# Kernel optimization log

Hardware: AMD Instinct MI355X
Metric: run time of the kernel (lower is better)

The kernel has to match this reference:

```python
import jax, jax.numpy as jnp
import numpy as np

# ---- constants (from init_kwargs / Box defaults) ----
B, K, T = 32768, 256, 10
C_LIGHT, F0, DF = 3.0e8, 1.0e10, 3.0e4
D_EL = C_LIGHT / (2.0 * F0)            # half-wavelength spacing
SPATIAL = F0 * D_EL / C_LIGHT          # = 0.5
RANGE_C = 2.0 * DF / C_LIGHT           # = 2e-4
THETA_MIN, THETA_MAX = -60.0, 60.0
R_MIN, R_MAX = 0.0, 2000.0
BETA = 2.0
STEP_CLIP = 0.1
INIT_ALPHA, INIT_LAMBDA = 0.01, 0.001
ALPHA_MIN, ALPHA_MAX = 1e-6, 0.2
LAM_MIN, LAM_MAX = 1e-6, 1.0
EPS = 1e-6


def _atanh(y):
    return jnp.arctanh(jnp.clip(y, -1.0 + EPS, 1.0 - EPS))


def map_theta_r_to_u(theta_deg, r_m):
    mid = 0.5 * (THETA_MIN + THETA_MAX)
    half = 0.5 * (THETA_MAX - THETA_MIN)
    y = (theta_deg - mid) / half
    s = jnp.clip((r_m - R_MIN) / (R_MAX - R_MIN), EPS, 1.0 - EPS)
    u_r = _atanh(2.0 * s - 1.0)          # tanh r_box inverse
    return jnp.stack([_atanh(y), u_r], axis=-1)  # (B,2)


def map_u_to_theta_r(u):
    mid = 0.5 * (THETA_MIN + THETA_MAX)
    half = 0.5 * (THETA_MAX - THETA_MIN)
    theta = mid + half * jnp.tanh(u[:, 0])
    s = 0.5 * (jnp.tanh(u[:, 1]) + 1.0)
    r = R_MIN + (R_MAX - R_MIN) * s
    return theta, r


def steering(theta_deg, r_m):
    # FDA steering: phase_k = 2*pi*k*(0.5*sin(theta) - 2*df*r/c)
    k = jnp.arange(K, dtype=jnp.float32)
    th = theta_deg * (jnp.pi / 180.0)
    phase = (2.0 * jnp.pi) * k[None, :] * (
        SPATIAL * jnp.sin(th)[:, None] - RANGE_C * r_m[:, None])  # (B,K)
    inv_sqrt_k = 1.0 / np.sqrt(K)
    return jnp.cos(phase) * inv_sqrt_k, jnp.sin(phase) * inv_sqrt_k


def loglike_logistic(theta_deg, r_m, z_re, z_im):
    # 1-bit logistic log-likelihood, summed over array elements -> (B,)
    a_re, a_im = steering(theta_deg, r_m)
    ll = jax.nn.log_sigmoid(BETA * z_re * a_re) + jax.nn.log_sigmoid(BETA * z_im * a_im)
    return jnp.sum(ll, axis=-1)


def setup_inputs() -> dict:
    key = jax.random.key(0)
    k1, k2, k3, k4 = jax.random.split(key, 4)
    z_real = jnp.sign(jax.random.normal(k1, (B, K), dtype=jnp.float32))
    z_imag = jnp.sign(jax.random.normal(k2, (B, K), dtype=jnp.float32))
    theta0 = jax.random.uniform(k3, (B,), jnp.float32, -55.0, 55.0)
    r0 = jax.random.uniform(k4, (B,), jnp.float32, 100.0, 1900.0)
    a_raw0 = float(np.log(np.expm1(INIT_ALPHA)))   # inverse softplus
    l_raw0 = float(np.log(np.expm1(INIT_LAMBDA)))
    return {
        "z_real": z_real, "z_imag": z_imag,
        "theta0_deg": theta0, "r0_m": r0,
        "alpha_theta_raw": jnp.full((T,), a_raw0, jnp.float32),
        "alpha_r_raw": jnp.full((T,), a_raw0, jnp.float32),
        "lambda_theta_raw": jnp.full((T,), l_raw0, jnp.float32),
        "lambda_r_raw": jnp.full((T,), l_raw0, jnp.float32),
    }


def reference(z_real, z_imag, theta0_deg, r0_m,
              alpha_theta_raw, alpha_r_raw, lambda_theta_raw, lambda_r_raw):
    alpha_th = jnp.clip(jax.nn.softplus(alpha_theta_raw), ALPHA_MIN, ALPHA_MAX)
    alpha_r = jnp.clip(jax.nn.softplus(alpha_r_raw), ALPHA_MIN, ALPHA_MAX)
    lam_th = jnp.clip(jax.nn.softplus(lambda_theta_raw), LAM_MIN, LAM_MAX)
    lam_r = jnp.clip(jax.nn.softplus(lambda_r_raw), LAM_MIN, LAM_MAX)

    u0 = map_theta_r_to_u(theta0_deg, r0_m)  # (B,2)

    def neg_obj_sum(u):
        th, r = map_u_to_theta_r(u)
        return -jnp.sum(loglike_logistic(th, r, z_real, z_imag))

    grad_fn = jax.grad(neg_obj_sum)

    def body(u, params):
        a_th, a_r, l_th, l_r = params
        # first-order unroll: gradient is a constant w.r.t. outer autodiff
        g = jax.lax.stop_gradient(grad_fn(u))
        g = jnp.where(jnp.isfinite(g), g, 0.0)
        g_th, g_r = g[:, 0], g[:, 1]
        a_th = jnp.where(jnp.isfinite(a_th), a_th, INIT_ALPHA)
        a_r = jnp.where(jnp.isfinite(a_r), a_r, INIT_ALPHA)
        l_th = jnp.where(jnp.isfinite(l_th), l_th, INIT_LAMBDA)
        l_r = jnp.where(jnp.isfinite(l_r), l_r, INIT_LAMBDA)
        den_th = jnp.maximum(jnp.nan_to_num(
            jnp.maximum(jnp.abs(g_th), 1e-6) + l_th, nan=1.0, posinf=1.0, neginf=1.0), 1e-6)
        den_r = jnp.maximum(jnp.nan_to_num(
            jnp.maximum(jnp.abs(g_r), 1e-6) + l_r, nan=1.0, posinf=1.0, neginf=1.0), 1e-6)
        step_u = jnp.stack([a_th * g_th / den_th, a_r * g_r / den_r], axis=-1)
        step_u = jnp.clip(jnp.nan_to_num(step_u, nan=0.0, posinf=0.0, neginf=0.0),
                          -STEP_CLIP, STEP_CLIP)
        return u - step_u, None

    uT, _ = jax.lax.scan(body, u0, (alpha_th, alpha_r, lam_th, lam_r))
    theta_T, r_T = map_u_to_theta_r(uT)
    return jnp.stack([theta_T, r_T], axis=-1)  # (B,2)
```

## Files before the change

### kernel.cpp

```cpp
#include <hip/hip_runtime.h>
#include <cstdint>

#define PI_F 3.14159265358979323846f

typedef float v2f __attribute__((ext_vector_type(2)));

__device__ __forceinline__ float fract_(float x)  { return __builtin_amdgcn_fractf(x); }
__device__ __forceinline__ float sin2pi_(float r) { return __builtin_amdgcn_sinf(r); }
__device__ __forceinline__ float cos2pi_(float r) { return __builtin_amdgcn_cosf(r); }
__device__ __forceinline__ v2f  splat2(float x)   { v2f r; r.x = x; r.y = x; return r; }

extern "C" __global__ void __launch_bounds__(256)
refine(const float* __restrict__ th0, const float* __restrict__ r0,
       const float* __restrict__ a_th_raw, const float* __restrict__ a_r_raw,
       const float* __restrict__ l_th_raw, const float* __restrict__ l_r_raw,
       const float4* __restrict__ zr4, const float4* __restrict__ zi4,
       float* __restrict__ out) {
    const int lane = threadIdx.x & 63;
    const int w    = threadIdx.x >> 6;
    const int il   = lane & 15;
    const int cw   = lane >> 4;
    const int item = blockIdx.x * 64 + w * 16 + il;

    __shared__ float sp[4][10];

    if (threadIdx.x < 40) {
        const int a = threadIdx.x / 10, i = threadIdx.x % 10;
        const float* src = (a == 0) ? a_th_raw : (a == 1) ? a_r_raw
                         : (a == 2) ? l_th_raw : l_r_raw;
        const float v  = log1pf(expf(src[i]));
        const float hi = (a < 2) ? 0.2f : 1.0f;
        sp[a][i] = fminf(fmaxf(v, 1e-6f), hi);
    }

    const float4* za = zr4 + (size_t)item * 64 + (size_t)cw * 16;
    const float4* zb = zi4 + (size_t)item * 64 + (size_t)cw * 16;
    uint32_t br0 = 0u, br1 = 0u, bi0 = 0u, bi1 = 0u;
    #pragma unroll
    for (int q = 0; q < 8; ++q) {
        const float4 a0 = za[q];
        const float4 a1 = za[q + 8];
        const float4 b0 = zb[q];
        const float4 b1 = zb[q + 8];
        br0 |= ((uint32_t)(a0.x < 0.f) << (4 * q))     | ((uint32_t)(a0.y < 0.f) << (4 * q + 1))
             | ((uint32_t)(a0.z < 0.f) << (4 * q + 2)) | ((uint32_t)(a0.w < 0.f) << (4 * q + 3));
        br1 |= ((uint32_t)(a1.x < 0.f) << (4 * q))     | ((uint32_t)(a1.y < 0.f) << (4 * q + 1))
             | ((uint32_t)(a1.z < 0.f) << (4 * q + 2)) | ((uint32_t)(a1.w < 0.f) << (4 * q + 3));
        bi0 |= ((uint32_t)(b0.x < 0.f) << (4 * q))     | ((uint32_t)(b0.y < 0.f) << (4 * q + 1))
             | ((uint32_t)(b0.z < 0.f) << (4 * q + 2)) | ((uint32_t)(b0.w < 0.f) << (4 * q + 3));
        bi1 |= ((uint32_t)(b1.x < 0.f) << (4 * q))     | ((uint32_t)(b1.y < 0.f) << (4 * q + 1))
             | ((uint32_t)(b1.z < 0.f) << (4 * q + 2)) | ((uint32_t)(b1.w < 0.f) << (4 * q + 3));
    }

    float y = th0[item] * (1.0f / 60.0f);
    y = fminf(fmaxf(y, -1.0f + 1e-6f), 1.0f - 1e-6f);
    float u0 = atanhf(y);
    float sR = r0[item] * (1.0f / 2000.0f);
    sR = fminf(fmaxf(sR, 1e-6f), 1.0f - 1e-6f);
    float u1 = atanhf(2.0f * sR - 1.0f);

    const float w64 = (float)(cw * 64);

    __syncthreads();

    for (int t = 0; t < 10; ++t) {
        const float ath = sp[0][t], ar = sp[1][t], lth = sp[2][t], lr = sp[3][t];

        const float T0 = tanhf(u0), T1 = tanhf(u1);
        const float th_rad = (PI_F / 3.0f) * T0;
        const float sth = sinf(th_rad), cth = cosf(th_rad);
        const float r   = 1000.0f * (T1 + 1.0f);
        const float crev = 0.5f * sth - 2e-4f * r;

        const float d4 = fract_(4.0f * crev);
        const v2f C4 = splat2(cos2pi_(d4));
        const v2f S4 = splat2(sin2pi_(d4));

        v2f c[2], s[2], kf[2], acc[2];
        #pragma unroll
        for (int p2 = 0; p2 < 2; ++p2) {
            const float k0a = w64 + (float)(2 * p2);
            const float k0b = w64 + (float)(2 * p2 + 1);
            const float rva = fract_(k0a * crev);
            const float rvb = fract_(k0b * crev);
            v2f cc, ssv, kk;
            cc.x  = cos2pi_(rva);  cc.y  = cos2pi_(rvb);
            ssv.x = sin2pi_(rva);  ssv.y = sin2pi_(rvb);
            kk.x  = k0a;           kk.y  = k0b;
            c[p2]   = cc;
            s[p2]   = ssv;
            kf[p2]  = kk;
            acc[p2] = splat2(0.0f);
        }

        const v2f mtwo = splat2(-2.0f);
        const v2f one  = splat2(1.0f);
        const v2f cub  = splat2(-(1.0f / 196608.0f));
        const v2f four = splat2(4.0f);

        #pragma unroll
        for (int j = 0; j < 16; ++j) {
            #pragma unroll
            for (int p2 = 0; p2 < 2; ++p2) {
                const int klA = 2 * p2 + 4 * j;
                const int klB = klA + 1;
                const uint32_t wr = (klA < 32) ? br0 : br1;
                const uint32_t wi = (klA < 32) ? bi0 : bi1;
                const uint32_t mreA = (wr << (31 - (klA & 31))) & 0x80000000u;
                const uint32_t mreB = (wr << (31 - (klB & 31))) & 0x80000000u;
                const uint32_t mimA = (wi << (31 - (klA & 31))) & 0x80000000u;
                const uint32_t mimB = (wi << (31 - (klB & 31))) & 0x80000000u;
                const v2f cs = c[p2], ss = s[p2];
                v2f zc, zs;
                zc.x = __uint_as_float(__float_as_uint(cs.x) ^ mimA);
                zc.y = __uint_as_float(__float_as_uint(cs.y) ^ mimB);
                zs.x = __uint_as_float(__float_as_uint(ss.x) ^ mreA);
                zs.y = __uint_as_float(__float_as_uint(ss.y) ^ mreB);
                const v2f w0 = zc - zs;
                const v2f u2 = ss * ss;
                const v2f t2 = __builtin_elementwise_fma(mtwo, u2, one);
                const v2f sc = ss * cs;
                const v2f v  = sc * t2;
                const v2f W  = __builtin_elementwise_fma(v, cub, w0 * 0.0625f);
                acc[p2] = __builtin_elementwise_fma(kf[p2], W, acc[p2]);
                kf[p2]  = kf[p2] + four;
                const v2f tA = ss * S4;
                const v2f tB = cs * S4;
                c[p2] = __builtin_elementwise_fma(cs, C4, -tA);
                s[p2] = __builtin_elementwise_fma(ss, C4, tB);
            }
        }
        float S = (acc[0].x + acc[0].y) + (acc[1].x + acc[1].y);

        S += __shfl_xor(S, 16, 64);
        S += __shfl_xor(S, 32, 64);

        const float g0 = -(PI_F * PI_F / 3.0f) * cth * (1.0f - T0 * T0) * S;
        const float g1 = 0.4f * PI_F * (1.0f - T1 * T1) * S;
        const float den0 = fmaxf(fabsf(g0), 1e-6f) + lth;
        const float den1 = fmaxf(fabsf(g1), 1e-6f) + lr;
        float st0 = ath * g0 / den0;
        float st1 = ar  * g1 / den1;
        st0 = fminf(fmaxf(st0, -0.1f), 0.1f);
        st1 = fminf(fmaxf(st1, -0.1f), 0.1f);
        u0 -= st0;
        u1 -= st1;
    }

    if (cw == 0) {
        const float thT = 60.0f * tanhf(u0);
        const float rT  = 1000.0f * (tanhf(u1) + 1.0f);
        reinterpret_cast<float2*>(out)[item] = make_float2(thT, rT);
    }
}

extern "C" void kernel_launch(void* const* d_in, const int* in_sizes, int n_in,
                              void* d_out, int out_size, void* d_ws, size_t ws_size,
                              hipStream_t stream) {
    const float* zr   = (const float*)d_in[0];
    const float* zi   = (const float*)d_in[1];
    const float* th0  = (const float*)d_in[2];
    const float* r0   = (const float*)d_in[3];
    const float* athr = (const float*)d_in[4];
    const float* arr  = (const float*)d_in[5];
    const float* lthr = (const float*)d_in[6];
    const float* lrr  = (const float*)d_in[7];

    const int B = in_sizes[2];

    refine<<<B / 64, 256, 0, stream>>>(th0, r0, athr, arr, lthr, lrr,
                                       (const float4*)zr, (const float4*)zi,
                                       (float*)d_out);
}
```

Measured before the change: 149.9 us.

## Pack sign bits in a separate ballot kernel and split items across more lanes

Adds a pre-pass kernel that reads z_real and z_imag with coalesced float4 loads and uses wavefront ballots to pack the sign bits into 32-bit words in workspace. The refine kernel then loads one packed word per lane and spreads each item over 8 lanes instead of 4, so each lane handles one pair of elements. This is meant to remove the strided per-thread float4 gather and raise parallelism. In exchange it adds a second launch, a workspace round trip, and an extra shuffle in the reduction.

```diff
diff --git a/kernel.cpp b/kernel.cpp
--- a/kernel.cpp
+++ b/kernel.cpp
@@ -11,16 +11,52 @@
 __device__ __forceinline__ v2f  splat2(float x)   { v2f r; r.x = x; r.y = x; return r; }
 
 extern "C" __global__ void __launch_bounds__(256)
+pack_signs(const float4* __restrict__ zr4, const float4* __restrict__ zi4,
+           uint32_t* __restrict__ pr, uint32_t* __restrict__ pim) {
+    const int lane = threadIdx.x & 63;
+    const int w    = threadIdx.x >> 6;
+    const int item = blockIdx.x * 4 + w;
+
+    const float4 fr = zr4[(size_t)item * 64 + lane];
+    const float4 fi = zi4[(size_t)item * 64 + lane];
+
+    const uint64_t Mr0 = __ballot(fr.x < 0.f);
+    const uint64_t Mr1 = __ballot(fr.y < 0.f);
+    const uint64_t Mr2 = __ballot(fr.z < 0.f);
+    const uint64_t Mr3 = __ballot(fr.w < 0.f);
+    const uint64_t Mi0 = __ballot(fi.x < 0.f);
+    const uint64_t Mi1 = __ballot(fi.y < 0.f);
+    const uint64_t Mi2 = __ballot(fi.z < 0.f);
+    const uint64_t Mi3 = __ballot(fi.w < 0.f);
+
+    if (lane < 16) {
+        const int comp = lane >> 3;
+        const int sub  = lane & 7;
+        const int cw   = sub >> 1;
+        const int h    = sub & 1;
+        const uint64_t ma = comp ? (h ? Mi2 : Mi0) : (h ? Mr2 : Mr0);
+        const uint64_t mb = comp ? (h ? Mi3 : Mi1) : (h ? Mr3 : Mr1);
+        const int sh = 16 * cw;
+        const uint32_t word = ((uint32_t)(ma >> sh) & 0xFFFFu)
+                            | (((uint32_t)(mb >> sh) & 0xFFFFu) << 16);
+        uint32_t* dst = comp ? pim : pr;
+        dst[(size_t)item * 8 + sub] = word;
+    }
+}
+
+extern "C" __global__ void __launch_bounds__(256)
 refine(const float* __restrict__ th0, const float* __restrict__ r0,
        const float* __restrict__ a_th_raw, const float* __restrict__ a_r_raw,
        const float* __restrict__ l_th_raw, const float* __restrict__ l_r_raw,
-       const float4* __restrict__ zr4, const float4* __restrict__ zi4,
+       const uint32_t* __restrict__ pr, const uint32_t* __restrict__ pim,
        float* __restrict__ out) {
     const int lane = threadIdx.x & 63;
     const int w    = threadIdx.x >> 6;
-    const int il   = lane & 15;
-    const int cw   = lane >> 4;
-    const int item = blockIdx.x * 64 + w * 16 + il;
+    const int il   = lane & 7;
+    const int sub  = lane >> 3;
+    const int cw   = sub >> 1;
+    const int h    = sub & 1;
+    const int item = blockIdx.x * 32 + w * 8 + il;
 
     __shared__ float sp[4][10];
 
@@ -33,24 +69,8 @@
         sp[a][i] = fminf(fmaxf(v, 1e-6f), hi);
     }
 
-    const float4* za = zr4 + (size_t)item * 64 + (size_t)cw * 16;
-    const float4* zb = zi4 + (size_t)item * 64 + (size_t)cw * 16;
-    uint32_t br0 = 0u, br1 = 0u, bi0 = 0u, bi1 = 0u;
-    #pragma unroll
-    for (int q = 0; q < 8; ++q) {
-        const float4 a0 = za[q];
-        const float4 a1 = za[q + 8];
-        const float4 b0 = zb[q];
-        const float4 b1 = zb[q + 8];
-        br0 |= ((uint32_t)(a0.x < 0.f) << (4 * q))     | ((uint32_t)(a0.y < 0.f) << (4 * q + 1))
-             | ((uint32_t)(a0.z < 0.f) << (4 * q + 2)) | ((uint32_t)(a0.w < 0.f) << (4 * q + 3));
-        br1 |= ((uint32_t)(a1.x < 0.f) << (4 * q))     | ((uint32_t)(a1.y < 0.f) << (4 * q + 1))
-             | ((uint32_t)(a1.z < 0.f) << (4 * q + 2)) | ((uint32_t)(a1.w < 0.f) << (4 * q + 3));
-        bi0 |= ((uint32_t)(b0.x < 0.f) << (4 * q))     | ((uint32_t)(b0.y < 0.f) << (4 * q + 1))
-             | ((uint32_t)(b0.z < 0.f) << (4 * q + 2)) | ((uint32_t)(b0.w < 0.f) << (4 * q + 3));
-        bi1 |= ((uint32_t)(b1.x < 0.f) << (4 * q))     | ((uint32_t)(b1.y < 0.f) << (4 * q + 1))
-             | ((uint32_t)(b1.z < 0.f) << (4 * q + 2)) | ((uint32_t)(b1.w < 0.f) << (4 * q + 3));
-    }
+    const uint32_t br = pr [(size_t)item * 8 + sub];
+    const uint32_t bi = pim[(size_t)item * 8 + sub];
 
     float y = th0[item] * (1.0f / 60.0f);
     y = fminf(fmaxf(y, -1.0f + 1e-6f), 1.0f - 1e-6f);
@@ -59,7 +79,8 @@
     sR = fminf(fmaxf(sR, 1e-6f), 1.0f - 1e-6f);
     float u1 = atanhf(2.0f * sR - 1.0f);
 
-    const float w64 = (float)(cw * 64);
+    const float k0a = (float)(cw * 64 + 2 * h);
+    const float k0b = (float)(cw * 64 + 2 * h + 1);
 
     __syncthreads();
 
@@ -76,22 +97,13 @@
         const v2f C4 = splat2(cos2pi_(d4));
         const v2f S4 = splat2(sin2pi_(d4));
 
-        v2f c[2], s[2], kf[2], acc[2];
-        #pragma unroll
-        for (int p2 = 0; p2 < 2; ++p2) {
-            const float k0a = w64 + (float)(2 * p2);
-            const float k0b = w64 + (float)(2 * p2 + 1);
-            const float rva = fract_(k0a * crev);
-            const float rvb = fract_(k0b * crev);
-            v2f cc, ssv, kk;
-            cc.x  = cos2pi_(rva);  cc.y  = cos2pi_(rvb);
-            ssv.x = sin2pi_(rva);  ssv.y = sin2pi_(rvb);
-            kk.x  = k0a;           kk.y  = k0b;
-            c[p2]   = cc;
-            s[p2]   = ssv;
-            kf[p2]  = kk;
-            acc[p2] = splat2(0.0f);
-        }
+        const float rva = fract_(k0a * crev);
+        const float rvb = fract_(k0b * crev);
+        v2f c, s, kf, acc;
+        c.x  = cos2pi_(rva);  c.y  = cos2pi_(rvb);
+        s.x  = sin2pi_(rva);  s.y  = sin2pi_(rvb);
+        kf.x = k0a;           kf.y = k0b;
+        acc  = splat2(0.0f);
 
         const v2f mtwo = splat2(-2.0f);
         const v2f one  = splat2(1.0f);
@@ -100,38 +112,31 @@
 
         #pragma unroll
         for (int j = 0; j < 16; ++j) {
-            #pragma unroll
-            for (int p2 = 0; p2 < 2; ++p2) {
-                const int klA = 2 * p2 + 4 * j;
-                const int klB = klA + 1;
-                const uint32_t wr = (klA < 32) ? br0 : br1;
-                const uint32_t wi = (klA < 32) ? bi0 : bi1;
-                const uint32_t mreA = (wr << (31 - (klA & 31))) & 0x80000000u;
-                const uint32_t mreB = (wr << (31 - (klB & 31))) & 0x80000000u;
-                const uint32_t mimA = (wi << (31 - (klA & 31))) & 0x80000000u;
-                const uint32_t mimB = (wi << (31 - (klB & 31))) & 0x80000000u;
-                const v2f cs = c[p2], ss = s[p2];
-                v2f zc, zs;
-                zc.x = __uint_as_float(__float_as_uint(cs.x) ^ mimA);
-                zc.y = __uint_as_float(__float_as_uint(cs.y) ^ mimB);
-                zs.x = __uint_as_float(__float_as_uint(ss.x) ^ mreA);
-                zs.y = __uint_as_float(__float_as_uint(ss.y) ^ mreB);
-                const v2f w0 = zc - zs;
-                const v2f u2 = ss * ss;
-                const v2f t2 = __builtin_elementwise_fma(mtwo, u2, one);
-                const v2f sc = ss * cs;
-                const v2f v  = sc * t2;
-                const v2f W  = __builtin_elementwise_fma(v, cub, w0 * 0.0625f);
-                acc[p2] = __builtin_elementwise_fma(kf[p2], W, acc[p2]);
-                kf[p2]  = kf[p2] + four;
-                const v2f tA = ss * S4;
-                const v2f tB = cs * S4;
-                c[p2] = __builtin_elementwise_fma(cs, C4, -tA);
-                s[p2] = __builtin_elementwise_fma(ss, C4, tB);
-            }
+            const uint32_t mreA = (br << (31 - j)) & 0x80000000u;
+            const uint32_t mreB = (br << (15 - j)) & 0x80000000u;
+            const uint32_t mimA = (bi << (31 - j)) & 0x80000000u;
+            const uint32_t mimB = (bi << (15 - j)) & 0x80000000u;
+            const v2f cs = c, ss = s;
+            v2f zc, zs;
+            zc.x = __uint_as_float(__float_as_uint(cs.x) ^ mimA);
+            zc.y = __uint_as_float(__float_as_uint(cs.y) ^ mimB);
+            zs.x = __uint_as_float(__float_as_uint(ss.x) ^ mreA);
+            zs.y = __uint_as_float(__float_as_uint(ss.y) ^ mreB);
+            const v2f w0 = zc - zs;
+            const v2f u2 = ss * ss;
+            const v2f t2 = __builtin_elementwise_fma(mtwo, u2, one);
+            const v2f sc = ss * cs;
+            const v2f v  = sc * t2;
+            const v2f W  = __builtin_elementwise_fma(v, cub, w0 * 0.0625f);
+            acc = __builtin_elementwise_fma(kf, W, acc);
+            kf  = kf + four;
+            const v2f tA = ss * S4;
+            const v2f tB = cs * S4;
+            c = __builtin_elementwise_fma(cs, C4, -tA);
+            s = __builtin_elementwise_fma(ss, C4, tB);
         }
-        float S = (acc[0].x + acc[0].y) + (acc[1].x + acc[1].y);
-
+        float S = acc.x + acc.y;
+        S += __shfl_xor(S, 8, 64);
         S += __shfl_xor(S, 16, 64);
         S += __shfl_xor(S, 32, 64);
 
@@ -147,7 +152,7 @@
         u1 -= st1;
     }
 
-    if (cw == 0) {
+    if (sub == 0) {
         const float thT = 60.0f * tanhf(u0);
         const float rT  = 1000.0f * (tanhf(u1) + 1.0f);
         reinterpret_cast<float2*>(out)[item] = make_float2(thT, rT);
@@ -168,7 +173,11 @@
 
     const int B = in_sizes[2];
 
-    refine<<<B / 64, 256, 0, stream>>>(th0, r0, athr, arr, lthr, lrr,
-                                       (const float4*)zr, (const float4*)zi,
-                                       (float*)d_out);
+    uint32_t* pr  = (uint32_t*)d_ws;
+    uint32_t* pim = pr + (size_t)B * 8;
+
+    pack_signs<<<B / 4, 256, 0, stream>>>((const float4*)zr, (const float4*)zi,
+                                          pr, pim);
+    refine<<<B / 32, 256, 0, stream>>>(th0, r0, athr, arr, lthr, lrr,
+                                       pr, pim, (float*)d_out);
 }
```

Result: faster. 140.4 us (-6.3%).
